# Kernel tuning notes

Measured on AMD Instinct MI355X. Metric: run time of the kernel, lower is better.

The kernel has to match this reference:

```python
import jax, jax.numpy as jnp
import numpy as np

HIDDEN = 1024   # hidden_dimensions (dim_in)
NUM_HEADS = 16
HEAD_DIM = 64   # dim_q == dim_k == output_dimensions per head
BATCH = 4
SEQ = 2048


def setup_inputs() -> dict:
    key = jax.random.key(0)
    ks = jax.random.split(key, 11)
    s = 1.0 / np.sqrt(HIDDEN)
    so = 1.0 / np.sqrt(NUM_HEADS * HEAD_DIM)
    return {
        "Q": jax.random.normal(ks[0], (BATCH, SEQ, HIDDEN), jnp.float32),
        "K": jax.random.normal(ks[1], (BATCH, SEQ, HIDDEN), jnp.float32),
        "V": jax.random.normal(ks[2], (BATCH, SEQ, HIDDEN), jnp.float32),
        # per-head projection weights stacked over the head axis
        "Wq": jax.random.uniform(ks[3], (NUM_HEADS, HIDDEN, HEAD_DIM), jnp.float32, -s, s),
        "bq": jax.random.uniform(ks[4], (NUM_HEADS, HEAD_DIM), jnp.float32, -s, s),
        "Wk": jax.random.uniform(ks[5], (NUM_HEADS, HIDDEN, HEAD_DIM), jnp.float32, -s, s),
        "bk": jax.random.uniform(ks[6], (NUM_HEADS, HEAD_DIM), jnp.float32, -s, s),
        "Wv": jax.random.uniform(ks[7], (NUM_HEADS, HIDDEN, HEAD_DIM), jnp.float32, -s, s),
        "bv": jax.random.uniform(ks[8], (NUM_HEADS, HEAD_DIM), jnp.float32, -s, s),
        # output projection: concat(num_heads*head_dim) -> hidden
        "Wo": jax.random.uniform(ks[9], (NUM_HEADS * HEAD_DIM, HIDDEN), jnp.float32, -so, so),
        "bo": jax.random.uniform(ks[10], (HIDDEN,), jnp.float32, -so, so),
    }


def reference(Q, K, V, Wq, bq, Wk, bk, Wv, bv, Wo, bo):
    # Per-head linear projections (batched over heads instead of Python loop)
    q = jnp.einsum("bsd,hdk->bhsk", Q, Wq) + bq[None, :, None, :]  # [B,H,S,dk]
    k = jnp.einsum("bsd,hdk->bhsk", K, Wk) + bk[None, :, None, :]
    v = jnp.einsum("bsd,hdk->bhsk", V, Wv) + bv[None, :, None, :]
    # Scaled dot-product attention
    scale = 1.0 / jnp.sqrt(jnp.asarray(k.shape[-1], q.dtype))
    scores = jnp.einsum("bhqk,bhsk->bhqs", q, k) * scale          # [B,H,S,S]
    attn = jax.nn.softmax(scores, axis=-1)
    o = jnp.einsum("bhqs,bhsk->bhqk", attn, v)                     # [B,H,S,dk]
    # Concatenate heads along the feature dim, then output linear
    B, H, S, dk = o.shape
    concat = jnp.transpose(o, (0, 2, 1, 3)).reshape(B, S, H * dk)  # [B,S,H*dk]
    return concat @ Wo + bo                                        # [B,S,HIDDEN]
```

## Files before the change

kernel.cpp:

```cpp
#include <hip/hip_runtime.h>
#include <hip/hip_bf16.h>
#include <stdint.h>

typedef unsigned short u16;
typedef uint32_t u32;
typedef __attribute__((ext_vector_type(4))) float f32x4;
typedef __attribute__((ext_vector_type(8))) short s8v;
typedef __attribute__((ext_vector_type(4))) unsigned short u16x4;
typedef __attribute__((ext_vector_type(2))) uint32_t u32x2;

#define SCALE_Q 0.18033688f

__device__ __forceinline__ u16 f2bf(float f) {
  union { float f; uint32_t u; } v; v.f = f;
  uint32_t r = v.u + 0x7fffu + ((v.u >> 16) & 1u);
  return (u16)(r >> 16);
}

__device__ __forceinline__ u32 pk2(float lo, float hi) {
  __hip_bfloat162 h = __float22bfloat162_rn(float2{lo, hi});
  union { __hip_bfloat162 h; u32 u; } c; c.h = h; return c.u;
}

__device__ __forceinline__ void gl16(const void* g, void* l) {
  __builtin_amdgcn_global_load_lds((const __attribute__((address_space(1))) u32*)g,
                                   (__attribute__((address_space(3))) u32*)l, 16, 0, 0);
}

__global__ __launch_bounds__(256) void k_conv3(const float* __restrict__ a, const float* __restrict__ b,
                                               const float* __restrict__ c, u16* __restrict__ oa,
                                               u16* __restrict__ ob, u16* __restrict__ oc) {
  int which = blockIdx.y;
  const float* in = which == 0 ? a : (which == 1 ? b : c);
  u16* out = which == 0 ? oa : (which == 1 ? ob : oc);
  int i = (blockIdx.x * 256 + threadIdx.x) * 4;
  float4 v = *(const float4*)(in + i);
  u16x4 o; o[0] = f2bf(v.x); o[1] = f2bf(v.y); o[2] = f2bf(v.z); o[3] = f2bf(v.w);
  *(u16x4*)(out + i) = o;
}

__global__ __launch_bounds__(256) void k_convW_t(const float* __restrict__ wq, const float* __restrict__ wk,
                                                 const float* __restrict__ wv, u16* __restrict__ oq,
                                                 u16* __restrict__ ok, u16* __restrict__ ov) {
  __shared__ float T[64][65];
  const int z = blockIdx.z, h = blockIdx.y, d0 = blockIdx.x * 64;
  const float* w = z == 0 ? wq : (z == 1 ? wk : wv);
  u16* o = z == 0 ? oq : (z == 1 ? ok : ov);
  const float scale = z == 0 ? SCALE_Q : 1.0f;
  const int t = threadIdx.x;
#pragma unroll
  for (int i = 0; i < 16; ++i) {
    int f = t + i * 256;
    T[f >> 6][f & 63] = w[(h * 1024 + d0 + (f >> 6)) * 64 + (f & 63)];
  }
  __syncthreads();
#pragma unroll
  for (int i = 0; i < 16; ++i) {
    int g = t + i * 256;
    o[(h * 64 + (g >> 6)) * 1024 + d0 + (g & 63)] = f2bf(T[g & 63][g >> 6] * scale);
  }
}

__global__ __launch_bounds__(256) void k_convWo_t(const float* __restrict__ w, u16* __restrict__ o) {
  __shared__ float T[64][65];
  const int n0 = blockIdx.x * 64, c0 = blockIdx.y * 64;
  const int t = threadIdx.x;
#pragma unroll
  for (int i = 0; i < 16; ++i) {
    int f = t + i * 256;
    T[f >> 6][f & 63] = w[(c0 + (f >> 6)) * 1024 + n0 + (f & 63)];
  }
  __syncthreads();
#pragma unroll
  for (int i = 0; i < 16; ++i) {
    int g = t + i * 256;
    o[(n0 + (g >> 6)) * 1024 + c0 + (g & 63)] = f2bf(T[g & 63][g >> 6]);
  }
}

__global__ __launch_bounds__(256) void k_gemm3(
    const u16* __restrict__ Aq, const u16* __restrict__ Ak, const u16* __restrict__ Av,
    const u16* __restrict__ Bq, const u16* __restrict__ Bk, const u16* __restrict__ Bv,
    const float* __restrict__ bqp, const float* __restrict__ bkp, const float* __restrict__ bvp,
    u16* __restrict__ oq, u16* __restrict__ ok, u16* __restrict__ ov) {
  constexpr int Kd = 1024, Nd = 1024;
  __shared__ alignas(16) u16 As[2][128 * 64];
  __shared__ alignas(16) u16 Bs[2][128 * 64];
  const int z = blockIdx.z;
  const u16* A = z == 0 ? Aq : (z == 1 ? Ak : Av);
  const u16* Bt = z == 0 ? Bq : (z == 1 ? Bk : Bv);
  const float* bias = z == 0 ? bqp : (z == 1 ? bkp : bvp);

  const int t = threadIdx.x;
  const int lane = t & 63;
  const int w = t >> 6;
  const int wm = w >> 1, wn = w & 1;
  const int lr = lane & 15, lg = lane >> 4;
  const long bm = blockIdx.x * 128, bn = blockIdx.y * 128;
  const int r8 = lane >> 3, c8 = lane & 7;
  const int chunk = c8 ^ r8;

  f32x4 acc[4][4] = {};
  const u16* Ap = A + (bm + w * 8 + r8) * (long)Kd + chunk * 8;
  const u16* Bp = Bt + (bn + w * 8 + r8) * (long)Kd + chunk * 8;

  auto GSTAGE = [&](u16* Asb, u16* Bsb, int kt) {
#pragma unroll
    for (int p = 0; p < 4; ++p) {
      gl16(Ap + (long)p * 32 * Kd + kt, Asb + (p * 32 + w * 8) * 64);
      gl16(Bp + (long)p * 32 * Kd + kt, Bsb + (p * 32 + w * 8) * 64);
    }
  };
  auto GCOMP = [&](const u16* Asb, const u16* Bsb) {
#pragma unroll
    for (int ks = 0; ks < 2; ++ks) {
      s8v af[4], bf[4];
#pragma unroll
      for (int i = 0; i < 4; ++i) {
        int arow = wm * 64 + i * 16 + lr;
        af[i] = *(const s8v*)(Asb + arow * 64 + (((ks * 4 + lg) ^ (arow & 7)) * 8));
        int brow = wn * 64 + i * 16 + lr;
        bf[i] = *(const s8v*)(Bsb + brow * 64 + (((ks * 4 + lg) ^ (brow & 7)) * 8));
      }
#pragma unroll
      for (int i = 0; i < 4; ++i)
#pragma unroll
        for (int j = 0; j < 4; ++j)
          acc[i][j] = __builtin_amdgcn_mfma_f32_16x16x32_bf16(af[i], bf[j], acc[i][j], 0, 0, 0);
    }
  };

  GSTAGE(As[0], Bs[0], 0);
  __syncthreads();
  for (int kt = 0; kt < Kd; kt += 128) {
    if (kt + 64 < Kd) GSTAGE(As[1], Bs[1], kt + 64);
    GCOMP(As[0], Bs[0]);
    __syncthreads();
    if (kt + 128 < Kd) GSTAGE(As[0], Bs[0], kt + 128);
    GCOMP(As[1], Bs[1]);
    __syncthreads();
  }

  const float bscale = z == 0 ? SCALE_Q : 1.0f;
  float bcol[4];
#pragma unroll
  for (int j = 0; j < 4; ++j) bcol[j] = bias[bn + wn * 64 + j * 16 + lr] * bscale;

  if (z < 2) {
    u16* C = z == 0 ? oq : ok;
#pragma unroll
    for (int i = 0; i < 4; ++i) {
      long m0 = bm + wm * 64 + i * 16 + lg * 4;
#pragma unroll
      for (int j = 0; j < 4; ++j) {
        long n = bn + wn * 64 + j * 16 + lr;
#pragma unroll
        for (int r = 0; r < 4; ++r)
          C[(m0 + r) * Nd + n] = f2bf(acc[i][j][r] + bcol[j]);
      }
    }
  } else {
    u16* C = ov;
#pragma unroll
    for (int i = 0; i < 4; ++i) {
      long m0 = bm + wm * 64 + i * 16 + lg * 4;
      int b = (int)(m0 >> 11), s0 = (int)(m0 & 2047);
#pragma unroll
      for (int j = 0; j < 4; ++j) {
        int n = (int)(bn + wn * 64 + j * 16 + lr);
        int h = n >> 6, dv = n & 63;
        u32x2 cc;
        cc[0] = pk2(acc[i][j][0] + bcol[j], acc[i][j][1] + bcol[j]);
        cc[1] = pk2(acc[i][j][2] + bcol[j], acc[i][j][3] + bcol[j]);
        *(u32x2*)(C + (long)((b * 16 + h) * 64 + dv) * 2048 + s0) = cc;
      }
    }
  }
}

__global__ __launch_bounds__(256) void k_gemmo(const u16* __restrict__ A, const u16* __restrict__ Bt,
                                               const float* __restrict__ bias, float* __restrict__ C) {
  constexpr int Kd = 1024, Nd = 1024;
  __shared__ alignas(16) u16 As[2][128 * 64];
  __shared__ alignas(16) u16 Bs[2][128 * 64];
  const int t = threadIdx.x;
  const int lane = t & 63;
  const int w = t >> 6;
  const int wm = w >> 1, wn = w & 1;
  const int lr = lane & 15, lg = lane >> 4;
  const long bm = blockIdx.x * 128, bn = blockIdx.y * 128;
  const int r8 = lane >> 3, c8 = lane & 7;
  const int chunk = c8 ^ r8;

  f32x4 acc[4][4] = {};
  const u16* Ap = A + (bm + w * 8 + r8) * (long)Kd + chunk * 8;
  const u16* Bp = Bt + (bn + w * 8 + r8) * (long)Kd + chunk * 8;

  auto GSTAGE = [&](u16* Asb, u16* Bsb, int kt) {
#pragma unroll
    for (int p = 0; p < 4; ++p) {
      gl16(Ap + (long)p * 32 * Kd + kt, Asb + (p * 32 + w * 8) * 64);
      gl16(Bp + (long)p * 32 * Kd + kt, Bsb + (p * 32 + w * 8) * 64);
    }
  };
  auto GCOMP = [&](const u16* Asb, const u16* Bsb) {
#pragma unroll
    for (int ks = 0; ks < 2; ++ks) {
      s8v af[4], bf[4];
#pragma unroll
      for (int i = 0; i < 4; ++i) {
        int arow = wm * 64 + i * 16 + lr;
        af[i] = *(const s8v*)(Asb + arow * 64 + (((ks * 4 + lg) ^ (arow & 7)) * 8));
        int brow = wn * 64 + i * 16 + lr;
        bf[i] = *(const s8v*)(Bsb + brow * 64 + (((ks * 4 + lg) ^ (brow & 7)) * 8));
      }
#pragma unroll
      for (int i = 0; i < 4; ++i)
#pragma unroll
        for (int j = 0; j < 4; ++j)
          acc[i][j] = __builtin_amdgcn_mfma_f32_16x16x32_bf16(af[i], bf[j], acc[i][j], 0, 0, 0);
    }
  };

  GSTAGE(As[0], Bs[0], 0);
  __syncthreads();
  for (int kt = 0; kt < Kd; kt += 128) {
    if (kt + 64 < Kd) GSTAGE(As[1], Bs[1], kt + 64);
    GCOMP(As[0], Bs[0]);
    __syncthreads();
    if (kt + 128 < Kd) GSTAGE(As[0], Bs[0], kt + 128);
    GCOMP(As[1], Bs[1]);
    __syncthreads();
  }

  float bcol[4];
#pragma unroll
  for (int j = 0; j < 4; ++j) bcol[j] = bias[bn + wn * 64 + j * 16 + lr];
#pragma unroll
  for (int i = 0; i < 4; ++i) {
    long m0 = bm + wm * 64 + i * 16 + lg * 4;
#pragma unroll
    for (int j = 0; j < 4; ++j) {
      long n = bn + wn * 64 + j * 16 + lr;
#pragma unroll
      for (int r = 0; r < 4; ++r)
        C[(m0 + r) * Nd + n] = acc[i][j][r] + bcol[j];
    }
  }
}

__global__ __launch_bounds__(512, 4) void k_attn(const u16* __restrict__ q, const u16* __restrict__ k,
                                                 const u16* __restrict__ vT, u16* __restrict__ o) {
  __shared__ alignas(16) u16 Ks[2][64 * 64];
  __shared__ alignas(16) u16 Vs[2][64 * 64];
  __shared__ alignas(16) u32 Pp[8 * 32 * 36];
  const int t = threadIdx.x;
  const int lane = t & 63;
  const int wv = t >> 6;
  const int lr = lane & 15, lg = lane >> 4;
  const int qt = blockIdx.x, h = blockIdx.y, b = blockIdx.z;
  const int r8 = lane >> 3, c8 = lane & 7;

  const int qbase = qt * 256 + wv * 32;
  const u16* qp0 = q + ((long)(b * 2048 + qbase + lr) * 1024 + h * 64);
  const u16* qp1 = qp0 + 16 * 1024;
  const s8v qf00 = *(const s8v*)(qp0 + lg * 8);
  const s8v qf01 = *(const s8v*)(qp0 + 32 + lg * 8);
  const s8v qf10 = *(const s8v*)(qp1 + lg * 8);
  const s8v qf11 = *(const s8v*)(qp1 + 32 + lg * 8);

  const u16* Kpp = k + (long)b * 2048 * 1024 + h * 64 + (long)(wv * 8 + r8) * 1024 + ((c8 ^ r8) * 8);
  const u16* Vpp = vT + (long)(b * 16 + h) * 131072 + (long)(wv * 8 + r8) * 2048 + ((c8 ^ r8) * 8);

  f32x4 acc0[4] = {}, acc1[4] = {};
  float l0 = 0.f, l1 = 0.f;
  u32* Pr0 = &Pp[(wv * 32 + lr) * 36];
  u32* Pr1 = Pr0 + 16 * 36;

  auto ASTAGE = [&](u16* ksd, u16* vsd, int kv) {
    gl16(Kpp + (long)kv * 1024, ksd + (wv * 8) * 64);
    gl16(Vpp + kv,              vsd + (wv * 8) * 64);
  };

  auto ATILE = [&](const u16* Ksb, const u16* Vsb) {
    f32x4 sa0[4], sa1[4];
#pragma unroll
    for (int mi = 0; mi < 4; ++mi) {
      int kr = mi * 16 + lr, rx = kr & 7;
      s8v k0 = *(const s8v*)(Ksb + kr * 64 + ((lg ^ rx) * 8));
      s8v k1 = *(const s8v*)(Ksb + kr * 64 + (((4 + lg) ^ rx) * 8));
      f32x4 z0 = {}, z1 = {};
      z0 = __builtin_amdgcn_mfma_f32_16x16x32_bf16(k0, qf00, z0, 0, 0, 0);
      z1 = __builtin_amdgcn_mfma_f32_16x16x32_bf16(k0, qf10, z1, 0, 0, 0);
      z0 = __builtin_amdgcn_mfma_f32_16x16x32_bf16(k1, qf01, z0, 0, 0, 0);
      z1 = __builtin_amdgcn_mfma_f32_16x16x32_bf16(k1, qf11, z1, 0, 0, 0);
      sa0[mi] = z0; sa1[mi] = z1;
    }
#pragma unroll
    for (int mi = 0; mi < 4; ++mi) {
      float p0 = __builtin_amdgcn_exp2f(sa0[mi][0]);
      float p1 = __builtin_amdgcn_exp2f(sa0[mi][1]);
      float p2 = __builtin_amdgcn_exp2f(sa0[mi][2]);
      float p3 = __builtin_amdgcn_exp2f(sa0[mi][3]);
      l0 += (p0 + p1) + (p2 + p3);
      u32x2 c0; c0[0] = pk2(p0, p1); c0[1] = pk2(p2, p3);
      *(u32x2*)(Pr0 + mi * 8 + lg * 2) = c0;
      float r0 = __builtin_amdgcn_exp2f(sa1[mi][0]);
      float r1 = __builtin_amdgcn_exp2f(sa1[mi][1]);
      float r2 = __builtin_amdgcn_exp2f(sa1[mi][2]);
      float r3 = __builtin_amdgcn_exp2f(sa1[mi][3]);
      l1 += (r0 + r1) + (r2 + r3);
      u32x2 c1; c1[0] = pk2(r0, r1); c1[1] = pk2(r2, r3);
      *(u32x2*)(Pr1 + mi * 8 + lg * 2) = c1;
    }
#pragma unroll
    for (int ks = 0; ks < 2; ++ks) {
      s8v pf0 = *(const s8v*)(Pr0 + ks * 16 + lg * 4);
      s8v pf1 = *(const s8v*)(Pr1 + ks * 16 + lg * 4);
#pragma unroll
      for (int mi = 0; mi < 4; ++mi) {
        int vr = mi * 16 + lr;
        s8v vf = *(const s8v*)(Vsb + vr * 64 + (((ks * 4 + lg) ^ (vr & 7)) * 8));
        acc0[mi] = __builtin_amdgcn_mfma_f32_16x16x32_bf16(vf, pf0, acc0[mi], 0, 0, 0);
        acc1[mi] = __builtin_amdgcn_mfma_f32_16x16x32_bf16(vf, pf1, acc1[mi], 0, 0, 0);
      }
    }
  };

  ASTAGE(Ks[0], Vs[0], 0);
  for (int kv = 0; kv < 2048; kv += 128) {
    __syncthreads();
    if (kv + 64 < 2048) ASTAGE(Ks[1], Vs[1], kv + 64);
    ATILE(Ks[0], Vs[0]);
    __syncthreads();
    if (kv + 128 < 2048) ASTAGE(Ks[0], Vs[0], kv + 128);
    ATILE(Ks[1], Vs[1]);
  }

  l0 += __shfl_xor(l0, 16); l0 += __shfl_xor(l0, 32);
  l1 += __shfl_xor(l1, 16); l1 += __shfl_xor(l1, 32);
  float i0 = 1.0f / l0, i1 = 1.0f / l1;
  u16* op0 = o + ((long)(b * 2048 + qbase + lr) * 1024 + h * 64);
  u16* op1 = op0 + 16 * 1024;
#pragma unroll
  for (int mi = 0; mi < 4; ++mi) {
    u32x2 c0, c1;
    c0[0] = pk2(acc0[mi][0] * i0, acc0[mi][1] * i0);
    c0[1] = pk2(acc0[mi][2] * i0, acc0[mi][3] * i0);
    *(u32x2*)(op0 + mi * 16 + lg * 4) = c0;
    c1[0] = pk2(acc1[mi][0] * i1, acc1[mi][1] * i1);
    c1[1] = pk2(acc1[mi][2] * i1, acc1[mi][3] * i1);
    *(u32x2*)(op1 + mi * 16 + lg * 4) = c1;
  }
}

extern "C" void kernel_launch(void* const* d_in, const int* in_sizes, int n_in,
                              void* d_out, int out_size, void* d_ws, size_t ws_size,
                              hipStream_t stream) {
  const float* Q  = (const float*)d_in[0];
  const float* K  = (const float*)d_in[1];
  const float* V  = (const float*)d_in[2];
  const float* Wq = (const float*)d_in[3];
  const float* bq = (const float*)d_in[4];
  const float* Wk = (const float*)d_in[5];
  const float* bk = (const float*)d_in[6];
  const float* Wv = (const float*)d_in[7];
  const float* bvp = (const float*)d_in[8];
  const float* Wo = (const float*)d_in[9];
  const float* bo = (const float*)d_in[10];
  float* out = (float*)d_out;

  char* ws = (char*)d_ws;
  const size_t MB16 = (size_t)8192 * 1024 * 2;
  u16* Qb  = (u16*)(ws);
  u16* Kb  = (u16*)(ws + MB16);
  u16* Vb  = (u16*)(ws + 2 * MB16);
  u16* WqT = (u16*)(ws + 3 * MB16);
  u16* WkT = (u16*)(ws + 3 * MB16 + ((size_t)2 << 20));
  u16* WvT = (u16*)(ws + 3 * MB16 + ((size_t)4 << 20));
  u16* WoT = (u16*)(ws + 3 * MB16 + ((size_t)6 << 20));
  u16* qws = (u16*)(ws + 3 * MB16 + ((size_t)8 << 20));
  u16* kws = (u16*)(ws + 4 * MB16 + ((size_t)8 << 20));
  u16* vTs = (u16*)(ws + 5 * MB16 + ((size_t)8 << 20));
  u16* ows = Qb;

  k_conv3<<<dim3(8192, 3), 256, 0, stream>>>(Q, K, V, Qb, Kb, Vb);
  k_convW_t<<<dim3(16, 16, 3), 256, 0, stream>>>(Wq, Wk, Wv, WqT, WkT, WvT);
  k_convWo_t<<<dim3(16, 16), 256, 0, stream>>>(Wo, WoT);

  k_gemm3<<<dim3(64, 8, 3), 256, 0, stream>>>(Qb, Kb, Vb, WqT, WkT, WvT,
                                              bq, bk, bvp, qws, kws, vTs);

  k_attn<<<dim3(8, 16, 4), 512, 0, stream>>>(qws, kws, vTs, ows);

  k_gemmo<<<dim3(64, 8), 256, 0, stream>>>(ows, WoT, bo, out);
}
```

Baseline: 209.2 us.

## Switch attention to 32x32x16 MFMA and keep P in registers

The attention kernel moves from 16x16x32 to 32x32x16 bf16 MFMA tiles. Because the score accumulator layout now lines up with the B-operand layout of the PV MFMA, the exponentiated probabilities are packed directly in registers instead of round-tripping through LDS. The V projection epilogue permutes its row ordering (lgp) so that vT matches the new key ordering. This removes the LDS writes and reads of P and reduces MFMA instruction count, at the cost of larger accumulator register footprints.

Result: slower. 219.2 us (+4.8%).

```diff
diff --git a/kernel.cpp b/kernel.cpp
--- a/kernel.cpp
+++ b/kernel.cpp
@@ -5,6 +5,7 @@
 typedef unsigned short u16;
 typedef uint32_t u32;
 typedef __attribute__((ext_vector_type(4))) float f32x4;
+typedef __attribute__((ext_vector_type(16))) float f32x16;
 typedef __attribute__((ext_vector_type(8))) short s8v;
 typedef __attribute__((ext_vector_type(4))) unsigned short u16x4;
 typedef __attribute__((ext_vector_type(2))) uint32_t u32x2;
@@ -161,9 +162,10 @@
     }
   } else {
     u16* C = ov;
+    int lgp = ((lg & 1) << 1) | (lg >> 1);
 #pragma unroll
     for (int i = 0; i < 4; ++i) {
-      long m0 = bm + wm * 64 + i * 16 + lg * 4;
+      long m0 = bm + wm * 64 + i * 16 + lgp * 4;
       int b = (int)(m0 >> 11), s0 = (int)(m0 & 2047);
 #pragma unroll
       for (int j = 0; j < 4; ++j) {
@@ -253,29 +255,25 @@
                                                  const u16* __restrict__ vT, u16* __restrict__ o) {
   __shared__ alignas(16) u16 Ks[2][64 * 64];
   __shared__ alignas(16) u16 Vs[2][64 * 64];
-  __shared__ alignas(16) u32 Pp[8 * 32 * 36];
   const int t = threadIdx.x;
   const int lane = t & 63;
   const int wv = t >> 6;
-  const int lr = lane & 15, lg = lane >> 4;
+  const int l5 = lane & 31, hi = lane >> 5;
   const int qt = blockIdx.x, h = blockIdx.y, b = blockIdx.z;
   const int r8 = lane >> 3, c8 = lane & 7;
-
-  const int qbase = qt * 256 + wv * 32;
-  const u16* qp0 = q + ((long)(b * 2048 + qbase + lr) * 1024 + h * 64);
-  const u16* qp1 = qp0 + 16 * 1024;
-  const s8v qf00 = *(const s8v*)(qp0 + lg * 8);
-  const s8v qf01 = *(const s8v*)(qp0 + 32 + lg * 8);
-  const s8v qf10 = *(const s8v*)(qp1 + lg * 8);
-  const s8v qf11 = *(const s8v*)(qp1 + 32 + lg * 8);
+  const int rx = l5 & 7;
+
+  const int qrow = qt * 256 + wv * 32 + l5;
+  const u16* qp = q + ((long)(b * 2048 + qrow) * 1024 + h * 64);
+  s8v qf[4];
+#pragma unroll
+  for (int s = 0; s < 4; ++s) qf[s] = *(const s8v*)(qp + s * 16 + hi * 8);
 
   const u16* Kpp = k + (long)b * 2048 * 1024 + h * 64 + (long)(wv * 8 + r8) * 1024 + ((c8 ^ r8) * 8);
   const u16* Vpp = vT + (long)(b * 16 + h) * 131072 + (long)(wv * 8 + r8) * 2048 + ((c8 ^ r8) * 8);
 
-  f32x4 acc0[4] = {}, acc1[4] = {};
-  float l0 = 0.f, l1 = 0.f;
-  u32* Pr0 = &Pp[(wv * 32 + lr) * 36];
-  u32* Pr1 = Pr0 + 16 * 36;
+  f32x16 acc0 = {}, acc1 = {};
+  float l_loc = 0.f;
 
   auto ASTAGE = [&](u16* ksd, u16* vsd, int kv) {
     gl16(Kpp + (long)kv * 1024, ksd + (wv * 8) * 64);
@@ -283,47 +281,39 @@
   };
 
   auto ATILE = [&](const u16* Ksb, const u16* Vsb) {
-    f32x4 sa0[4], sa1[4];
-#pragma unroll
-    for (int mi = 0; mi < 4; ++mi) {
-      int kr = mi * 16 + lr, rx = kr & 7;
-      s8v k0 = *(const s8v*)(Ksb + kr * 64 + ((lg ^ rx) * 8));
-      s8v k1 = *(const s8v*)(Ksb + kr * 64 + (((4 + lg) ^ rx) * 8));
-      f32x4 z0 = {}, z1 = {};
-      z0 = __builtin_amdgcn_mfma_f32_16x16x32_bf16(k0, qf00, z0, 0, 0, 0);
-      z1 = __builtin_amdgcn_mfma_f32_16x16x32_bf16(k0, qf10, z1, 0, 0, 0);
-      z0 = __builtin_amdgcn_mfma_f32_16x16x32_bf16(k1, qf01, z0, 0, 0, 0);
-      z1 = __builtin_amdgcn_mfma_f32_16x16x32_bf16(k1, qf11, z1, 0, 0, 0);
-      sa0[mi] = z0; sa1[mi] = z1;
-    }
-#pragma unroll
-    for (int mi = 0; mi < 4; ++mi) {
-      float p0 = __builtin_amdgcn_exp2f(sa0[mi][0]);
-      float p1 = __builtin_amdgcn_exp2f(sa0[mi][1]);
-      float p2 = __builtin_amdgcn_exp2f(sa0[mi][2]);
-      float p3 = __builtin_amdgcn_exp2f(sa0[mi][3]);
-      l0 += (p0 + p1) + (p2 + p3);
-      u32x2 c0; c0[0] = pk2(p0, p1); c0[1] = pk2(p2, p3);
-      *(u32x2*)(Pr0 + mi * 8 + lg * 2) = c0;
-      float r0 = __builtin_amdgcn_exp2f(sa1[mi][0]);
-      float r1 = __builtin_amdgcn_exp2f(sa1[mi][1]);
-      float r2 = __builtin_amdgcn_exp2f(sa1[mi][2]);
-      float r3 = __builtin_amdgcn_exp2f(sa1[mi][3]);
-      l1 += (r0 + r1) + (r2 + r3);
-      u32x2 c1; c1[0] = pk2(r0, r1); c1[1] = pk2(r2, r3);
-      *(u32x2*)(Pr1 + mi * 8 + lg * 2) = c1;
-    }
-#pragma unroll
-    for (int ks = 0; ks < 2; ++ks) {
-      s8v pf0 = *(const s8v*)(Pr0 + ks * 16 + lg * 4);
-      s8v pf1 = *(const s8v*)(Pr1 + ks * 16 + lg * 4);
-#pragma unroll
-      for (int mi = 0; mi < 4; ++mi) {
-        int vr = mi * 16 + lr;
-        s8v vf = *(const s8v*)(Vsb + vr * 64 + (((ks * 4 + lg) ^ (vr & 7)) * 8));
-        acc0[mi] = __builtin_amdgcn_mfma_f32_16x16x32_bf16(vf, pf0, acc0[mi], 0, 0, 0);
-        acc1[mi] = __builtin_amdgcn_mfma_f32_16x16x32_bf16(vf, pf1, acc1[mi], 0, 0, 0);
-      }
+    f32x16 sa0 = {}, sa1 = {};
+#pragma unroll
+    for (int s = 0; s < 4; ++s) {
+      int cw = 2 * s + hi;
+      s8v kf0 = *(const s8v*)(Ksb + l5 * 64 + ((cw ^ rx) * 8));
+      s8v kf1 = *(const s8v*)(Ksb + (32 + l5) * 64 + ((cw ^ rx) * 8));
+      sa0 = __builtin_amdgcn_mfma_f32_32x32x16_bf16(kf0, qf[s], sa0, 0, 0, 0);
+      sa1 = __builtin_amdgcn_mfma_f32_32x32x16_bf16(kf1, qf[s], sa1, 0, 0, 0);
+    }
+    u32 Ppk[16];
+#pragma unroll
+    for (int kb = 0; kb < 2; ++kb) {
+#pragma unroll
+      for (int r1 = 0; r1 < 4; ++r1) {
+        float p0 = __builtin_amdgcn_exp2f(kb ? sa1[4 * r1 + 0] : sa0[4 * r1 + 0]);
+        float p1 = __builtin_amdgcn_exp2f(kb ? sa1[4 * r1 + 1] : sa0[4 * r1 + 1]);
+        float p2 = __builtin_amdgcn_exp2f(kb ? sa1[4 * r1 + 2] : sa0[4 * r1 + 2]);
+        float p3 = __builtin_amdgcn_exp2f(kb ? sa1[4 * r1 + 3] : sa0[4 * r1 + 3]);
+        l_loc += (p0 + p1) + (p2 + p3);
+        Ppk[kb * 8 + r1 * 2 + 0] = pk2(p0, p1);
+        Ppk[kb * 8 + r1 * 2 + 1] = pk2(p2, p3);
+      }
+    }
+#pragma unroll
+    for (int s2 = 0; s2 < 4; ++s2) {
+      union { s8v v; u32 w[4]; } pu;
+      pu.w[0] = Ppk[4 * s2 + 0]; pu.w[1] = Ppk[4 * s2 + 1];
+      pu.w[2] = Ppk[4 * s2 + 2]; pu.w[3] = Ppk[4 * s2 + 3];
+      int cw = 2 * s2 + hi;
+      s8v vf0 = *(const s8v*)(Vsb + l5 * 64 + ((cw ^ rx) * 8));
+      s8v vf1 = *(const s8v*)(Vsb + (32 + l5) * 64 + ((cw ^ rx) * 8));
+      acc0 = __builtin_amdgcn_mfma_f32_32x32x16_bf16(vf0, pu.v, acc0, 0, 0, 0);
+      acc1 = __builtin_amdgcn_mfma_f32_32x32x16_bf16(vf1, pu.v, acc1, 0, 0, 0);
     }
   };
 
@@ -337,20 +327,22 @@
     ATILE(Ks[1], Vs[1]);
   }
 
-  l0 += __shfl_xor(l0, 16); l0 += __shfl_xor(l0, 32);
-  l1 += __shfl_xor(l1, 16); l1 += __shfl_xor(l1, 32);
-  float i0 = 1.0f / l0, i1 = 1.0f / l1;
-  u16* op0 = o + ((long)(b * 2048 + qbase + lr) * 1024 + h * 64);
-  u16* op1 = op0 + 16 * 1024;
-#pragma unroll
-  for (int mi = 0; mi < 4; ++mi) {
-    u32x2 c0, c1;
-    c0[0] = pk2(acc0[mi][0] * i0, acc0[mi][1] * i0);
-    c0[1] = pk2(acc0[mi][2] * i0, acc0[mi][3] * i0);
-    *(u32x2*)(op0 + mi * 16 + lg * 4) = c0;
-    c1[0] = pk2(acc1[mi][0] * i1, acc1[mi][1] * i1);
-    c1[1] = pk2(acc1[mi][2] * i1, acc1[mi][3] * i1);
-    *(u32x2*)(op1 + mi * 16 + lg * 4) = c1;
+  l_loc += __shfl_xor(l_loc, 32);
+  float inv = 1.0f / l_loc;
+  u16* op = o + ((long)(b * 2048 + qrow) * 1024 + h * 64);
+#pragma unroll
+  for (int kb = 0; kb < 2; ++kb) {
+#pragma unroll
+    for (int r1 = 0; r1 < 4; ++r1) {
+      u32x2 cc;
+      float a0 = kb ? acc1[4 * r1 + 0] : acc0[4 * r1 + 0];
+      float a1 = kb ? acc1[4 * r1 + 1] : acc0[4 * r1 + 1];
+      float a2 = kb ? acc1[4 * r1 + 2] : acc0[4 * r1 + 2];
+      float a3 = kb ? acc1[4 * r1 + 3] : acc0[4 * r1 + 3];
+      cc[0] = pk2(a0 * inv, a1 * inv);
+      cc[1] = pk2(a2 * inv, a3 * inv);
+      *(u32x2*)(op + kb * 32 + r1 * 8 + hi * 4) = cc;
+    }
   }
 }
 
```
